# Optimization experiments

Hardware: AMD Instinct MI355X
Metric: run time of the kernel (lower is better)

The kernel has to match this reference:

```python
import jax, jax.numpy as jnp
import numpy as np

B, T, S, E = 16, 1024, 1024, 1024  # note: module requires T == E (see bmm shape constraint)


def setup_inputs() -> dict:
    key = jax.random.key(0)
    ks = jax.random.split(key, 11)
    w = lambda k: jax.random.normal(k, (E, E), dtype=jnp.float32) * 0.02
    b = lambda k: jax.random.normal(k, (E,), dtype=jnp.float32) * 0.02
    return {
        "query": jax.random.normal(ks[0], (B, T, E), dtype=jnp.float32),
        "key": jax.random.normal(ks[1], (B, S, E), dtype=jnp.float32),
        "value": jax.random.normal(ks[2], (B, S, E), dtype=jnp.float32),
        "Wq": w(ks[3]), "bq": b(ks[4]),
        "Wk": w(ks[5]), "bk": b(ks[6]),
        "Wv": w(ks[7]), "bv": b(ks[8]),
        "Wo": w(ks[9]), "bo": b(ks[10]),
    }


def reference(query, key, value, Wq, bq, Wk, bk, Wv, bv, Wo, bo):
    # torch Linear: y = x @ W.T + b
    q = query @ Wq.T + bq          # [B, T, E]
    k = key @ Wk.T + bk            # [B, S, E]
    v = value @ Wv.T + bv          # [B, S, E]
    # Faithful to source: BOTH q and k are transposed to [B, E, len] before bmm,
    # so weights[b, i, s] = sum_t q[b, t, i] * k[b, s, t]  (requires T == E).
    scale = 1.0 / jnp.sqrt(jnp.asarray(q.shape[-1], q.dtype))
    w = jnp.einsum('bti,bst->bis', q, k) * scale   # [B, E, S]
    a = jax.nn.softmax(w, axis=-1)                 # softmax over src_len
    o = jnp.einsum('bis,bse->bie', a, v)           # [B, E, E]
    return o @ Wo.T + bo
```

## Files before the change

kernel.cpp:

```cpp
#include <hip/hip_runtime.h>
#include <hip/hip_bf16.h>
#include <stdint.h>

typedef __attribute__((ext_vector_type(8))) short short8;
typedef __attribute__((ext_vector_type(4))) float floatx4;

#define MODE_PROJ_T 0
#define MODE_PROJ_N 1
#define MODE_SCORES 2
#define MODE_ATT    3
#define MODE_OUT    4

__device__ __forceinline__ unsigned short f2bf(float f) {
    union { float f; unsigned int u; } x; x.f = f;
    unsigned int u = x.u + 0x7FFFu + ((x.u >> 16) & 1u);
    return (unsigned short)(u >> 16);
}

__device__ __forceinline__ void gload_lds16(const void* g, void* lds) {
    __builtin_amdgcn_global_load_lds(
        (const __attribute__((address_space(1))) unsigned int*)g,
        (__attribute__((address_space(3))) unsigned int*)lds,
        16, 0, 0);
}

template<int MODE>
__global__ __launch_bounds__(256) void gemm_nt(
    const __hip_bfloat16* __restrict__ A,
    const __hip_bfloat16* __restrict__ Bm,
    const float* __restrict__ bias,
    void* __restrict__ Cout,
    int K, long sA, long sB, long sC, float alpha)
{
    __shared__ short As[128 * 64];
    __shared__ short Bs[128 * 64];

    const int tid  = threadIdx.x;
    const int wid  = tid >> 6;
    const int lane = tid & 63;

    const int id  = blockIdx.x;
    const int xcd = id & 7;
    const int s   = id >> 3;
    int bx, by, bz;
    if (MODE == MODE_SCORES || MODE == MODE_ATT) {
        bz = xcd + ((s >> 6) << 3);
        by = (s >> 3) & 7;
        bx = s & 7;
    } else {
        bz = 0;
        bx = s >> 4;
        by = ((s & 15) << 3) | xcd;
    }
    const int row0 = by * 128;
    const int col0 = bx * 128;

    const __hip_bfloat16* Ab = A  + (size_t)bz * sA;
    const __hip_bfloat16* Bb = Bm + (size_t)bz * sB;

    floatx4 acc[4][4];
#pragma unroll
    for (int i = 0; i < 4; i++)
#pragma unroll
        for (int j = 0; j < 4; j++) acc[i][j] = (floatx4){0.f, 0.f, 0.f, 0.f};

    const int l7   = lane & 7;
    const int l3   = lane >> 3;
    const int cblk = ((l7 ^ l3) << 3);
    const int wm   = wid >> 1, wn = wid & 1;
    const int l15  = lane & 15, quad = lane >> 4;

    for (int k0 = 0; k0 < K; k0 += 64) {
        __syncthreads();
#pragma unroll
        for (int i = 0; i < 4; i++) {
            const int c = wid * 4 + i;
            const int r = c * 8 + l3;
            gload_lds16(Ab + (size_t)(row0 + r) * 1024 + k0 + cblk, As + c * 512);
            gload_lds16(Bb + (size_t)(col0 + r) * 1024 + k0 + cblk, Bs + c * 512);
        }
        __syncthreads();
#pragma unroll
        for (int ks = 0; ks < 2; ks++) {
            short8 af[4], bfr[4];
            const int kb = (((ks * 4 + quad) ^ l7) << 3);
#pragma unroll
            for (int t = 0; t < 4; t++) {
                af[t]  = *(const short8*)&As[(wm * 64 + t * 16 + l15) * 64 + kb];
                bfr[t] = *(const short8*)&Bs[(wn * 64 + t * 16 + l15) * 64 + kb];
            }
#pragma unroll
            for (int mt = 0; mt < 4; mt++)
#pragma unroll
                for (int nt = 0; nt < 4; nt++)
                    acc[mt][nt] = __builtin_amdgcn_mfma_f32_16x16x32_bf16(
                        af[mt], bfr[nt], acc[mt][nt], 0, 0, 0);
        }
    }

#pragma unroll
    for (int nt = 0; nt < 4; nt++) {
        const int col = col0 + wn * 64 + nt * 16 + l15;
        float bv = 0.f;
        if (MODE == MODE_PROJ_T || MODE == MODE_PROJ_N || MODE == MODE_OUT) bv = bias[col];
#pragma unroll
        for (int mt = 0; mt < 4; mt++) {
            const int rbase = row0 + wm * 64 + mt * 16 + quad * 4;
#pragma unroll
            for (int r = 0; r < 4; r++) {
                const int m = rbase + r;
                float v = acc[mt][nt][r];
                if (MODE == MODE_SCORES) v *= alpha;
                v += bv;
                if (MODE == MODE_SCORES) {
                    ((float*)Cout)[(size_t)bz * sC + (size_t)m * 1024 + col] = v;
                } else if (MODE == MODE_OUT) {
                    ((float*)Cout)[(size_t)m * 1024 + col] = v;
                } else if (MODE == MODE_PROJ_N || MODE == MODE_ATT) {
                    ((unsigned short*)Cout)[(size_t)bz * sC + (size_t)m * 1024 + col] = f2bf(v);
                } else {
                    ((unsigned short*)Cout)[((size_t)(m >> 10) << 20) + (size_t)col * 1024 + (m & 1023)] = f2bf(v);
                }
            }
        }
    }
}

__global__ __launch_bounds__(256) void softmax_rows(
    const float* __restrict__ S, unsigned short* __restrict__ A)
{
    const int row  = blockIdx.x * 4 + (threadIdx.x >> 6);
    const int lane = threadIdx.x & 63;
    const float4* p = (const float4*)(S + (size_t)row * 1024);
    float4 v[4];
    float mx = -3.0e38f;
#pragma unroll
    for (int i = 0; i < 4; i++) {
        v[i] = p[lane + i * 64];
        mx = fmaxf(mx, fmaxf(fmaxf(v[i].x, v[i].y), fmaxf(v[i].z, v[i].w)));
    }
#pragma unroll
    for (int off = 32; off >= 1; off >>= 1) mx = fmaxf(mx, __shfl_xor(mx, off, 64));
    float e[16], sum = 0.f;
#pragma unroll
    for (int i = 0; i < 4; i++) {
        e[i*4+0] = __expf(v[i].x - mx); e[i*4+1] = __expf(v[i].y - mx);
        e[i*4+2] = __expf(v[i].z - mx); e[i*4+3] = __expf(v[i].w - mx);
        sum += e[i*4+0] + e[i*4+1] + e[i*4+2] + e[i*4+3];
    }
#pragma unroll
    for (int off = 32; off >= 1; off >>= 1) sum += __shfl_xor(sum, off, 64);
    const float inv = 1.0f / sum;
    ushort4* out = (ushort4*)(A + (size_t)row * 1024);
#pragma unroll
    for (int i = 0; i < 4; i++) {
        ushort4 o;
        o.x = f2bf(e[i*4+0] * inv); o.y = f2bf(e[i*4+1] * inv);
        o.z = f2bf(e[i*4+2] * inv); o.w = f2bf(e[i*4+3] * inv);
        out[lane + i * 64] = o;
    }
}

__global__ __launch_bounds__(256) void cvt_all(
    const float* __restrict__ q, const float* __restrict__ k, const float* __restrict__ v,
    const float* __restrict__ wq, const float* __restrict__ wk,
    const float* __restrict__ wv, const float* __restrict__ wo,
    unsigned short* __restrict__ qb, unsigned short* __restrict__ kb, unsigned short* __restrict__ vb,
    unsigned short* __restrict__ wqb, unsigned short* __restrict__ wkb,
    unsigned short* __restrict__ wvb, unsigned short* __restrict__ wob)
{
    const int id = blockIdx.x;
    const float* src; unsigned short* dst; int base;
    if      (id < 16384) { src = q;  dst = qb;  base = 0; }
    else if (id < 32768) { src = k;  dst = kb;  base = 16384; }
    else if (id < 49152) { src = v;  dst = vb;  base = 32768; }
    else if (id < 50176) { src = wq; dst = wqb; base = 49152; }
    else if (id < 51200) { src = wk; dst = wkb; base = 50176; }
    else if (id < 52224) { src = wv; dst = wvb; base = 51200; }
    else                 { src = wo; dst = wob; base = 52224; }
    const int i = (id - base) * 256 + threadIdx.x;
    const float4 vv = ((const float4*)src)[i];
    ushort4 o; o.x = f2bf(vv.x); o.y = f2bf(vv.y); o.z = f2bf(vv.z); o.w = f2bf(vv.w);
    ((ushort4*)dst)[i] = o;
}

extern "C" void kernel_launch(void* const* d_in, const int* in_sizes, int n_in,
                              void* d_out, int out_size, void* d_ws, size_t ws_size,
                              hipStream_t stream) {
    const float* query = (const float*)d_in[0];
    const float* key   = (const float*)d_in[1];
    const float* value = (const float*)d_in[2];
    const float* Wq = (const float*)d_in[3];  const float* bq = (const float*)d_in[4];
    const float* Wk = (const float*)d_in[5];  const float* bk = (const float*)d_in[6];
    const float* Wv = (const float*)d_in[7];  const float* bv = (const float*)d_in[8];
    const float* Wo = (const float*)d_in[9];  const float* bo = (const float*)d_in[10];

    char* ws = (char*)d_ws;
    const size_t MB = 1ull << 20;
    unsigned short* qbf = (unsigned short*)(ws + 0   * MB);
    unsigned short* kbf = (unsigned short*)(ws + 32  * MB);
    unsigned short* vbf = (unsigned short*)(ws + 64  * MB);
    unsigned short* wqb = (unsigned short*)(ws + 96  * MB);
    unsigned short* wkb = (unsigned short*)(ws + 98  * MB);
    unsigned short* wvb = (unsigned short*)(ws + 100 * MB);
    unsigned short* wob = (unsigned short*)(ws + 102 * MB);
    unsigned short* qT  = (unsigned short*)(ws + 104 * MB);
    unsigned short* kp  = (unsigned short*)(ws + 136 * MB);
    unsigned short* vT  = (unsigned short*)(ws + 168 * MB);
    float*          sc  = (float*)(ws + 0 * MB);
    unsigned short* att = (unsigned short*)(ws + 64 * MB);
    unsigned short* ob  = (unsigned short*)(ws + 104 * MB);

    const long S1M = 1 << 20;
    dim3 blk(256);

    cvt_all<<<53248, blk, 0, stream>>>(query, key, value, Wq, Wk, Wv, Wo,
                                       qbf, kbf, vbf, wqb, wkb, wvb, wob);

    gemm_nt<MODE_PROJ_T><<<1024, blk, 0, stream>>>(
        (const __hip_bfloat16*)qbf, (const __hip_bfloat16*)wqb, bq, qT, 1024, 0, 0, 0, 1.f);
    gemm_nt<MODE_PROJ_N><<<1024, blk, 0, stream>>>(
        (const __hip_bfloat16*)kbf, (const __hip_bfloat16*)wkb, bk, kp, 1024, 0, 0, 0, 1.f);
    gemm_nt<MODE_PROJ_T><<<1024, blk, 0, stream>>>(
        (const __hip_bfloat16*)vbf, (const __hip_bfloat16*)wvb, bv, vT, 1024, 0, 0, 0, 1.f);

    gemm_nt<MODE_SCORES><<<1024, blk, 0, stream>>>(
        (const __hip_bfloat16*)qT, (const __hip_bfloat16*)kp, nullptr, sc, 1024,
        S1M, S1M, S1M, 0.03125f);

    softmax_rows<<<4096, blk, 0, stream>>>(sc, att);

    gemm_nt<MODE_ATT><<<1024, blk, 0, stream>>>(
        (const __hip_bfloat16*)att, (const __hip_bfloat16*)vT, nullptr, ob, 1024,
        S1M, S1M, S1M, 1.f);

    gemm_nt<MODE_OUT><<<1024, blk, 0, stream>>>(
        (const __hip_bfloat16*)ob, (const __hip_bfloat16*)wob, bo, d_out, 1024, 0, 0, 0, 1.f);
}
```

Before: 543.4 us.

## Fuse Q/K/V projections into one launch and widen conversion kernel

Merges the three projection GEMMs into a single 3072-block launch. Each block picks its segment (Q, K or V) from its column tile and selects the matching input, weight, bias and output layout. The fp32-to-bf16 conversion now writes one packed buffer and has each thread convert 8 elements per iteration over 4 iterations, which cuts the block count. The goal is to remove launch gaps and tail effects between the projections and to make the conversion more efficient. The price is a workspace layout where segment offsets must line up exactly.

```diff
diff --git a/kernel.cpp b/kernel.cpp
--- a/kernel.cpp
+++ b/kernel.cpp
@@ -5,8 +5,7 @@
 typedef __attribute__((ext_vector_type(8))) short short8;
 typedef __attribute__((ext_vector_type(4))) float floatx4;
 
-#define MODE_PROJ_T 0
-#define MODE_PROJ_N 1
+#define MODE_QKV    0
 #define MODE_SCORES 2
 #define MODE_ATT    3
 #define MODE_OUT    4
@@ -29,6 +28,8 @@
     const __hip_bfloat16* __restrict__ A,
     const __hip_bfloat16* __restrict__ Bm,
     const float* __restrict__ bias,
+    const float* __restrict__ bias2,
+    const float* __restrict__ bias3,
     void* __restrict__ Cout,
     int K, long sA, long sB, long sC, float alpha)
 {
@@ -54,9 +55,20 @@
     }
     const int row0 = by * 128;
     const int col0 = bx * 128;
-
-    const __hip_bfloat16* Ab = A  + (size_t)bz * sA;
-    const __hip_bfloat16* Bb = Bm + (size_t)bz * sB;
+    const int seg  = (MODE == MODE_QKV) ? (bx >> 3) : 0;
+
+    const __hip_bfloat16* Ab;
+    const __hip_bfloat16* Bb;
+    int colA0;
+    if (MODE == MODE_QKV) {
+        Ab = A  + ((size_t)seg << 24);
+        Bb = Bm + ((size_t)seg << 20);
+        colA0 = col0 & 1023;
+    } else {
+        Ab = A  + (size_t)bz * sA;
+        Bb = Bm + (size_t)bz * sB;
+        colA0 = col0;
+    }
 
     floatx4 acc[4][4];
 #pragma unroll
@@ -77,7 +89,7 @@
             const int c = wid * 4 + i;
             const int r = c * 8 + l3;
             gload_lds16(Ab + (size_t)(row0 + r) * 1024 + k0 + cblk, As + c * 512);
-            gload_lds16(Bb + (size_t)(col0 + r) * 1024 + k0 + cblk, Bs + c * 512);
+            gload_lds16(Bb + (size_t)(colA0 + r) * 1024 + k0 + cblk, Bs + c * 512);
         }
         __syncthreads();
 #pragma unroll
@@ -101,8 +113,14 @@
 #pragma unroll
     for (int nt = 0; nt < 4; nt++) {
         const int col = col0 + wn * 64 + nt * 16 + l15;
+        const int cl  = col & 1023;
         float bv = 0.f;
-        if (MODE == MODE_PROJ_T || MODE == MODE_PROJ_N || MODE == MODE_OUT) bv = bias[col];
+        if (MODE == MODE_QKV) {
+            const float* bp = (seg == 0) ? bias : ((seg == 1) ? bias2 : bias3);
+            bv = bp[cl];
+        } else if (MODE == MODE_OUT) {
+            bv = bias[col];
+        }
 #pragma unroll
         for (int mt = 0; mt < 4; mt++) {
             const int rbase = row0 + wm * 64 + mt * 16 + quad * 4;
@@ -116,10 +134,15 @@
                     ((float*)Cout)[(size_t)bz * sC + (size_t)m * 1024 + col] = v;
                 } else if (MODE == MODE_OUT) {
                     ((float*)Cout)[(size_t)m * 1024 + col] = v;
-                } else if (MODE == MODE_PROJ_N || MODE == MODE_ATT) {
+                } else if (MODE == MODE_ATT) {
                     ((unsigned short*)Cout)[(size_t)bz * sC + (size_t)m * 1024 + col] = f2bf(v);
                 } else {
-                    ((unsigned short*)Cout)[((size_t)(m >> 10) << 20) + (size_t)col * 1024 + (m & 1023)] = f2bf(v);
+                    unsigned short* o = (unsigned short*)Cout + ((size_t)seg << 24);
+                    if (seg == 1) {
+                        o[(size_t)m * 1024 + cl] = f2bf(v);
+                    } else {
+                        o[((size_t)(m >> 10) << 20) + (size_t)cl * 1024 + (m & 1023)] = f2bf(v);
+                    }
                 }
             }
         }
@@ -165,23 +188,30 @@
     const float* __restrict__ q, const float* __restrict__ k, const float* __restrict__ v,
     const float* __restrict__ wq, const float* __restrict__ wk,
     const float* __restrict__ wv, const float* __restrict__ wo,
-    unsigned short* __restrict__ qb, unsigned short* __restrict__ kb, unsigned short* __restrict__ vb,
-    unsigned short* __restrict__ wqb, unsigned short* __restrict__ wkb,
-    unsigned short* __restrict__ wvb, unsigned short* __restrict__ wob)
+    unsigned short* __restrict__ dst)
 {
-    const int id = blockIdx.x;
-    const float* src; unsigned short* dst; int base;
-    if      (id < 16384) { src = q;  dst = qb;  base = 0; }
-    else if (id < 32768) { src = k;  dst = kb;  base = 16384; }
-    else if (id < 49152) { src = v;  dst = vb;  base = 32768; }
-    else if (id < 50176) { src = wq; dst = wqb; base = 49152; }
-    else if (id < 51200) { src = wk; dst = wkb; base = 50176; }
-    else if (id < 52224) { src = wv; dst = wvb; base = 51200; }
-    else                 { src = wo; dst = wob; base = 52224; }
-    const int i = (id - base) * 256 + threadIdx.x;
-    const float4 vv = ((const float4*)src)[i];
-    ushort4 o; o.x = f2bf(vv.x); o.y = f2bf(vv.y); o.z = f2bf(vv.z); o.w = f2bf(vv.w);
-    ((ushort4*)dst)[i] = o;
+    const int id = blockIdx.x, t = threadIdx.x;
+    const float* src; int local; size_t dbase;
+    if      (id < 2048) { src = q;  local = id;        dbase = 0; }
+    else if (id < 4096) { src = k;  local = id - 2048; dbase = (size_t)16 << 20 >> 3; }
+    else if (id < 6144) { src = v;  local = id - 4096; dbase = (size_t)32 << 20 >> 3; }
+    else if (id < 6272) { src = wq; local = id - 6144; dbase = (size_t)48 << 20 >> 3; }
+    else if (id < 6400) { src = wk; local = id - 6272; dbase = (size_t)49 << 20 >> 3; }
+    else if (id < 6528) { src = wv; local = id - 6400; dbase = (size_t)50 << 20 >> 3; }
+    else                { src = wo; local = id - 6528; dbase = (size_t)51 << 20 >> 3; }
+    const float4* s4 = (const float4*)src + (size_t)local * 2048;
+    short8* d8 = (short8*)dst + dbase + (size_t)local * 1024;
+#pragma unroll
+    for (int j = 0; j < 4; j++) {
+        const float4 a = s4[j * 512 + 2 * t];
+        const float4 b = s4[j * 512 + 2 * t + 1];
+        short8 o;
+        o[0] = (short)f2bf(a.x); o[1] = (short)f2bf(a.y);
+        o[2] = (short)f2bf(a.z); o[3] = (short)f2bf(a.w);
+        o[4] = (short)f2bf(b.x); o[5] = (short)f2bf(b.y);
+        o[6] = (short)f2bf(b.z); o[7] = (short)f2bf(b.w);
+        d8[j * 256 + t] = o;
+    }
 }
 
 extern "C" void kernel_launch(void* const* d_in, const int* in_sizes, int n_in,
@@ -198,42 +228,34 @@
     char* ws = (char*)d_ws;
     const size_t MB = 1ull << 20;
     unsigned short* qbf = (unsigned short*)(ws + 0   * MB);
-    unsigned short* kbf = (unsigned short*)(ws + 32  * MB);
-    unsigned short* vbf = (unsigned short*)(ws + 64  * MB);
     unsigned short* wqb = (unsigned short*)(ws + 96  * MB);
-    unsigned short* wkb = (unsigned short*)(ws + 98  * MB);
-    unsigned short* wvb = (unsigned short*)(ws + 100 * MB);
-    unsigned short* wob = (unsigned short*)(ws + 102 * MB);
     unsigned short* qT  = (unsigned short*)(ws + 104 * MB);
+    float*          sc  = (float*)(ws + 0 * MB);
+    unsigned short* att = (unsigned short*)(ws + 64 * MB);
     unsigned short* kp  = (unsigned short*)(ws + 136 * MB);
     unsigned short* vT  = (unsigned short*)(ws + 168 * MB);
-    float*          sc  = (float*)(ws + 0 * MB);
-    unsigned short* att = (unsigned short*)(ws + 64 * MB);
     unsigned short* ob  = (unsigned short*)(ws + 104 * MB);
 
     const long S1M = 1 << 20;
     dim3 blk(256);
 
-    cvt_all<<<53248, blk, 0, stream>>>(query, key, value, Wq, Wk, Wv, Wo,
-                                       qbf, kbf, vbf, wqb, wkb, wvb, wob);
-
-    gemm_nt<MODE_PROJ_T><<<1024, blk, 0, stream>>>(
-        (const __hip_bfloat16*)qbf, (const __hip_bfloat16*)wqb, bq, qT, 1024, 0, 0, 0, 1.f);
-    gemm_nt<MODE_PROJ_N><<<1024, blk, 0, stream>>>(
-        (const __hip_bfloat16*)kbf, (const __hip_bfloat16*)wkb, bk, kp, 1024, 0, 0, 0, 1.f);
-    gemm_nt<MODE_PROJ_T><<<1024, blk, 0, stream>>>(
-        (const __hip_bfloat16*)vbf, (const __hip_bfloat16*)wvb, bv, vT, 1024, 0, 0, 0, 1.f);
+    cvt_all<<<6656, blk, 0, stream>>>(query, key, value, Wq, Wk, Wv, Wo, qbf);
+
+    gemm_nt<MODE_QKV><<<3072, blk, 0, stream>>>(
+        (const __hip_bfloat16*)qbf, (const __hip_bfloat16*)wqb, bq, bk, bv,
+        qT, 1024, 0, 0, 0, 1.f);
 
     gemm_nt<MODE_SCORES><<<1024, blk, 0, stream>>>(
-        (const __hip_bfloat16*)qT, (const __hip_bfloat16*)kp, nullptr, sc, 1024,
-        S1M, S1M, S1M, 0.03125f);
+        (const __hip_bfloat16*)qT, (const __hip_bfloat16*)kp, nullptr, nullptr, nullptr,
+        sc, 1024, S1M, S1M, S1M, 0.03125f);
 
     softmax_rows<<<4096, blk, 0, stream>>>(sc, att);
 
     gemm_nt<MODE_ATT><<<1024, blk, 0, stream>>>(
-        (const __hip_bfloat16*)att, (const __hip_bfloat16*)vT, nullptr, ob, 1024,
-        S1M, S1M, S1M, 1.f);
+        (const __hip_bfloat16*)att, (const __hip_bfloat16*)vT, nullptr, nullptr, nullptr,
+        ob, 1024, S1M, S1M, S1M, 1.f);
 
     gemm_nt<MODE_OUT><<<1024, blk, 0, stream>>>(
-        (const __hip_bfloat16*)ob, (const __hip_bfloat16*)wob, bo, d_out, 1024, 0, 0, 0, 1.f);
-}
+        (const __hip_bfloat16*)ob, (const __hip_bfloat16*)wqb + (3ull << 20), bo, nullptr, nullptr,
+        d_out, 1024, 0, 0, 0, 1.f);
+}
```

Result: slower. 582.7 us (+7.2%).
